# Kernel tuning notes

Measured on AMD Instinct MI355X. Metric: run time of the kernel, lower is better.

## Reference

```python
import jax, jax.numpy as jnp
import numpy as np

NUM_FIELDS = 64
# itertools.combinations(range(n), 2) order == row-major upper-triangle (k=1)
_IU, _JU = np.triu_indices(NUM_FIELDS, k=1)
_IU = jnp.asarray(_IU)
_JU = jnp.asarray(_JU)


def setup_inputs() -> dict:
    key = jax.random.key(0)
    inputs = jax.random.normal(key, (16384, NUM_FIELDS, 32), dtype=jnp.float32)
    return {"inputs": inputs}


def reference(inputs) -> jnp.ndarray:
    # Gram matrix of field embeddings per sample: [B, F, F]
    gram = jnp.einsum("bfd,bgd->bfg", inputs, inputs)
    # Upper-triangle (i<j) pairs, same order as itertools.combinations: [B, F*(F-1)/2]
    return gram[:, _IU, _JU]
```

## Files before the change

kernel.cpp:

```cpp
#include <hip/hip_runtime.h>

#define NF 64
#define ND 32
#define NPAIR 2016
#define XSTR 68
#define SAMP_FLOATS (ND * XSTR)

__global__ __launch_bounds__(256, 4) void ip_gram_kernel(
    const float* __restrict__ in, float* __restrict__ out) {

    __shared__ float smem[4 * SAMP_FLOATS];

    const int t = threadIdx.x;
    const int w = t >> 6;
    const int l = t & 63;
    const int s = blockIdx.x * 4 + w;

    float* xt = smem + w * SAMP_FLOATS;
    const float* src = in + (size_t)s * (NF * ND);

    #pragma unroll
    for (int it = 0; it < 8; ++it) {
        int idx4 = l + (it << 6);
        float4 v = ((const float4*)src)[idx4];
        int f  = idx4 >> 3;
        int d0 = (idx4 & 7) << 2;
        xt[(d0 + 0) * XSTR + f] = v.x;
        xt[(d0 + 1) * XSTR + f] = v.y;
        xt[(d0 + 2) * XSTR + f] = v.z;
        xt[(d0 + 3) * XSTR + f] = v.w;
    }
    __syncthreads();

    const int tx = l & 7;
    const int ty = l >> 3;
    float acc[8][8];
    #pragma unroll
    for (int r = 0; r < 8; ++r)
        #pragma unroll
        for (int c = 0; c < 8; ++c) acc[r][c] = 0.f;

    #pragma unroll 8
    for (int d = 0; d < ND; ++d) {
        const float* row = xt + d * XSTR;
        float4 a0 = *(const float4*)(row + (ty << 3));
        float4 a1 = *(const float4*)(row + (ty << 3) + 4);
        float4 b0 = *(const float4*)(row + (tx << 3));
        float4 b1 = *(const float4*)(row + (tx << 3) + 4);
        float a[8] = {a0.x, a0.y, a0.z, a0.w, a1.x, a1.y, a1.z, a1.w};
        float b[8] = {b0.x, b0.y, b0.z, b0.w, b1.x, b1.y, b1.z, b1.w};
        #pragma unroll
        for (int r = 0; r < 8; ++r)
            #pragma unroll
            for (int c = 0; c < 8; ++c)
                acc[r][c] += a[r] * b[c];
    }
    __syncthreads();

    float* g = xt;
    #pragma unroll
    for (int r = 0; r < 8; ++r) {
        int i  = (ty << 3) + r;
        int P0 = ((i * (127 - i)) >> 1) - i - 1 + (tx << 3);
        #pragma unroll
        for (int c = 0; c < 8; ++c) {
            int j = (tx << 3) + c;
            if (j > i) g[P0 + c] = acc[r][c];
        }
    }
    __syncthreads();

    float* dst = out + (size_t)s * NPAIR;
    #pragma unroll
    for (int k = 0; k < 8; ++k) {
        int idx4 = (k << 6) + l;
        if (idx4 < 504) {
            float4 v = *(const float4*)(g + (idx4 << 2));
            *(float4*)(dst + (idx4 << 2)) = v;
        }
    }
}

extern "C" void kernel_launch(void* const* d_in, const int* in_sizes, int n_in,
                              void* d_out, int out_size, void* d_ws, size_t ws_size,
                              hipStream_t stream) {
    const float* in = (const float*)d_in[0];
    float* out = (float*)d_out;
    const int nsamples = in_sizes[0] / (NF * ND);
    ip_gram_kernel<<<nsamples / 4, 256, 0, stream>>>(in, out);
}
```

Measured before the change: 234.0 us.

## Compute per-sample Gram matrix with bf16x3 MFMA instead of FP32 FMA

Result: no change. 233.0 us (-0.4%).

```diff
diff --git a/kernel.cpp b/kernel.cpp
--- a/kernel.cpp
+++ b/kernel.cpp
@@ -3,20 +3,25 @@
 #define NF 64
 #define ND 32
 #define NPAIR 2016
-#define XSTR 68
-#define SAMP_FLOATS (ND * XSTR)
+#define KSTR 40
+#define SAMP_BF (NF * KSTR)
 
-__global__ __launch_bounds__(256, 4) void ip_gram_kernel(
+typedef __attribute__((ext_vector_type(8))) short bf16x8;
+typedef __attribute__((ext_vector_type(4))) float f32x4;
+
+__global__ __launch_bounds__(256, 4) void ip_gram_mfma(
     const float* __restrict__ in, float* __restrict__ out) {
 
-    __shared__ float smem[4 * SAMP_FLOATS];
+    __shared__ unsigned short sh[4 * 2 * SAMP_BF];
 
     const int t = threadIdx.x;
     const int w = t >> 6;
     const int l = t & 63;
     const int s = blockIdx.x * 4 + w;
 
-    float* xt = smem + w * SAMP_FLOATS;
+    unsigned short* __restrict__ xhi = sh + w * 2 * SAMP_BF;
+    unsigned short* __restrict__ xlo = xhi + SAMP_BF;
+
     const float* src = in + (size_t)s * (NF * ND);
 
     #pragma unroll
@@ -24,59 +29,51 @@
         int idx4 = l + (it << 6);
         float4 v = ((const float4*)src)[idx4];
         int f  = idx4 >> 3;
-        int d0 = (idx4 & 7) << 2;
-        xt[(d0 + 0) * XSTR + f] = v.x;
-        xt[(d0 + 1) * XSTR + f] = v.y;
-        xt[(d0 + 2) * XSTR + f] = v.z;
-        xt[(d0 + 3) * XSTR + f] = v.w;
+        int k0 = (idx4 & 7) << 2;
+        float xv[4] = {v.x, v.y, v.z, v.w};
+        ushort4 hv, lv;
+        unsigned short* hp = (unsigned short*)&hv;
+        unsigned short* lp = (unsigned short*)&lv;
+        #pragma unroll
+        for (int e = 0; e < 4; ++e) {
+            unsigned xb = __builtin_bit_cast(unsigned, xv[e]);
+            hp[e] = (unsigned short)(xb >> 16);
+            float hf = __builtin_bit_cast(float, xb & 0xFFFF0000u);
+            float lf = xv[e] - hf;
+            lp[e] = (unsigned short)(__builtin_bit_cast(unsigned, lf) >> 16);
+        }
+        *(ushort4*)&xhi[f * KSTR + k0] = hv;
+        *(ushort4*)&xlo[f * KSTR + k0] = lv;
     }
-    __syncthreads();
 
-    const int tx = l & 7;
-    const int ty = l >> 3;
-    float acc[8][8];
+    const int q = l >> 4;
+    const int m = l & 15;
+    bf16x8 fhi[4], flo[4];
     #pragma unroll
-    for (int r = 0; r < 8; ++r)
-        #pragma unroll
-        for (int c = 0; c < 8; ++c) acc[r][c] = 0.f;
-
-    #pragma unroll 8
-    for (int d = 0; d < ND; ++d) {
-        const float* row = xt + d * XSTR;
-        float4 a0 = *(const float4*)(row + (ty << 3));
-        float4 a1 = *(const float4*)(row + (ty << 3) + 4);
-        float4 b0 = *(const float4*)(row + (tx << 3));
-        float4 b1 = *(const float4*)(row + (tx << 3) + 4);
-        float a[8] = {a0.x, a0.y, a0.z, a0.w, a1.x, a1.y, a1.z, a1.w};
-        float b[8] = {b0.x, b0.y, b0.z, b0.w, b1.x, b1.y, b1.z, b1.w};
-        #pragma unroll
-        for (int r = 0; r < 8; ++r)
-            #pragma unroll
-            for (int c = 0; c < 8; ++c)
-                acc[r][c] += a[r] * b[c];
+    for (int r = 0; r < 4; ++r) {
+        int off = (r * 16 + m) * KSTR + (q << 3);
+        fhi[r] = *(const bf16x8*)&xhi[off];
+        flo[r] = *(const bf16x8*)&xlo[off];
     }
-    __syncthreads();
-
-    float* g = xt;
-    #pragma unroll
-    for (int r = 0; r < 8; ++r) {
-        int i  = (ty << 3) + r;
-        int P0 = ((i * (127 - i)) >> 1) - i - 1 + (tx << 3);
-        #pragma unroll
-        for (int c = 0; c < 8; ++c) {
-            int j = (tx << 3) + c;
-            if (j > i) g[P0 + c] = acc[r][c];
-        }
-    }
-    __syncthreads();
 
     float* dst = out + (size_t)s * NPAIR;
     #pragma unroll
-    for (int k = 0; k < 8; ++k) {
-        int idx4 = (k << 6) + l;
-        if (idx4 < 504) {
-            float4 v = *(const float4*)(g + (idx4 << 2));
-            *(float4*)(dst + (idx4 << 2)) = v;
+    for (int ti = 0; ti < 4; ++ti) {
+        #pragma unroll
+        for (int tj = ti; tj < 4; ++tj) {
+            f32x4 c = {0.f, 0.f, 0.f, 0.f};
+            c = __builtin_amdgcn_mfma_f32_16x16x32_bf16(fhi[ti], fhi[tj], c, 0, 0, 0);
+            c = __builtin_amdgcn_mfma_f32_16x16x32_bf16(fhi[ti], flo[tj], c, 0, 0, 0);
+            c = __builtin_amdgcn_mfma_f32_16x16x32_bf16(flo[ti], fhi[tj], c, 0, 0, 0);
+            int j = tj * 16 + m;
+            #pragma unroll
+            for (int r = 0; r < 4; ++r) {
+                int i = ti * 16 + (q << 2) + r;
+                if (ti < tj || j > i) {
+                    int p = ((i * (127 - i)) >> 1) + j - i - 1;
+                    dst[p] = c[r];
+                }
+            }
         }
     }
 }
@@ -87,5 +84,5 @@
     const float* in = (const float*)d_in[0];
     float* out = (float*)d_out;
     const int nsamples = in_sizes[0] / (NF * ND);
-    ip_gram_kernel<<<nsamples / 4, 256, 0, stream>>>(in, out);
+    ip_gram_mfma<<<nsamples / 4, 256, 0, stream>>>(in, out);
 }
```
